# Optimization experiments

Measured on AMD Instinct MI355X. Metric: run time of the kernel, lower is better.

Reference implementation:

```python
import jax, jax.numpy as jnp
import numpy as np

DIM = 1024
CODEBOOK_SIZE = 8192
Z_SHAPE = (16, 4096, DIM)


def setup_inputs() -> dict:
    key = jax.random.key(0)
    k_z, k_cb = jax.random.split(key)
    z = jax.random.normal(k_z, Z_SHAPE, dtype=jnp.float32)
    # nn.Parameter(torch.rand(dim, codebook_size)) -> uniform [0, 1)
    codebook = jax.random.uniform(k_cb, (DIM, CODEBOOK_SIZE), dtype=jnp.float32)
    return {"z": z, "codebook": codebook}


def reference(z, codebook):
    prev_shape = z.shape
    dim = codebook.shape[0]
    z2 = z.reshape(-1, dim)                      # [N, dim]
    dotp = z2 @ codebook                         # [N, K]
    idxes = jnp.argmin(dotp, axis=1)             # [N]
    quantized = codebook.T[idxes]                # [N, dim] gather of codebook columns
    return quantized.reshape(prev_shape)
```

## Files before the change

### kernel.cpp

```cpp
#include <hip/hip_runtime.h>
#include <hip/hip_bf16.h>

#define M_ROWS 65536
#define N_COLS 8192
#define K_DIM  1024
#define CAP    64
#define MARGIN 0.5f
#define PRUNE  0.5f
#define NSEG   3

typedef __attribute__((ext_vector_type(8))) short bf16x8;
typedef __attribute__((ext_vector_type(4))) float f32x4;

__device__ __forceinline__ unsigned short f32_to_bf16_rne(float f) {
  unsigned int u = __float_as_uint(f);
  unsigned int r = u + 0x7fffu + ((u >> 16) & 1u);
  return (unsigned short)(r >> 16);
}

__global__ void vq_convert_z(const float* __restrict__ z, unsigned short* __restrict__ zb,
                             int* __restrict__ counts) {
  const int tid    = blockIdx.x * blockDim.x + threadIdx.x;
  const int stride = gridDim.x * blockDim.x;
  if (tid < M_ROWS) counts[tid] = 0;
  const int total = M_ROWS * (K_DIM / 4);
  for (int i = tid; i < total; i += stride) {
    float4 v = ((const float4*)z)[i];
    ushort4 o;
    o.x = f32_to_bf16_rne(v.x);
    o.y = f32_to_bf16_rne(v.y);
    o.z = f32_to_bf16_rne(v.z);
    o.w = f32_to_bf16_rne(v.w);
    ((ushort4*)zb)[i] = o;
  }
}

__global__ void vq_transpose_cb(const float* __restrict__ cb,
                                float* __restrict__ cbT,
                                unsigned short* __restrict__ cbTb) {
  __shared__ float tile[32][33];
  int n0 = blockIdx.x * 32;
  int k0 = blockIdx.y * 32;
  int tx = threadIdx.x;
  int ty = threadIdx.y;
#pragma unroll
  for (int i = 0; i < 4; ++i) {
    int k = k0 + ty + i * 8;
    tile[ty + i * 8][tx] = cb[(size_t)k * N_COLS + n0 + tx];
  }
  __syncthreads();
#pragma unroll
  for (int i = 0; i < 4; ++i) {
    int n = n0 + ty + i * 8;
    float v = tile[tx][ty + i * 8];
    cbT[(size_t)n * K_DIM + k0 + tx] = v;
    cbTb[(size_t)n * K_DIM + k0 + tx] = f32_to_bf16_rne(v);
  }
}

__global__ __launch_bounds__(256, 3) void vq_gemm(const unsigned short* __restrict__ zb,
                                                  const unsigned short* __restrict__ cbTb,
                                                  int* __restrict__ counts,
                                                  unsigned short* __restrict__ cand,
                                                  float* __restrict__ candv) {
  __shared__ __align__(16) unsigned short As[128 * 64];
  __shared__ __align__(16) unsigned short Bs[128 * 64];
  const int tid  = threadIdx.x;
  const int wave = tid >> 6;
  const int lane = tid & 63;
  const int quad = lane >> 4;
  const int l16  = lane & 15;
  const int b      = blockIdx.x;
  const int seg    = b >> 9;
  const int stripe = b & 511;
  const int row0 = stripe * 128;
  const int rr = lane >> 3;
  const int sgo = (((lane & 7) ^ rr) << 3);
  const int swz = l16 & 7;

  float run[2][4];
#pragma unroll
  for (int a = 0; a < 2; ++a)
#pragma unroll
    for (int b2 = 0; b2 < 4; ++b2) run[a][b2] = 1e30f;

  const int nc0 = (seg * 64) / NSEG;
  const int nc1 = ((seg + 1) * 64) / NSEG;
  for (int nc = nc0; nc < nc1; ++nc) {
    const int col0 = nc * 128;
    f32x4 acc[2][8];
#pragma unroll
    for (int a = 0; a < 2; ++a)
#pragma unroll
      for (int b2 = 0; b2 < 8; ++b2) acc[a][b2] = (f32x4){0.f, 0.f, 0.f, 0.f};

    for (int kk = 0; kk < K_DIM; kk += 64) {
      const int rbase = wave * 32;
#pragma unroll
      for (int c = 0; c < 4; ++c) {
        const int r = rbase + c * 8;
        const unsigned short* ga = zb + ((size_t)(row0 + r + rr) << 10) + kk + sgo;
        __builtin_amdgcn_global_load_lds(
            (const __attribute__((address_space(1))) void*)ga,
            (__attribute__((address_space(3))) void*)(As + r * 64), 16, 0, 0);
        const unsigned short* gb = cbTb + ((size_t)(col0 + r + rr) << 10) + kk + sgo;
        __builtin_amdgcn_global_load_lds(
            (const __attribute__((address_space(1))) void*)gb,
            (__attribute__((address_space(3))) void*)(Bs + r * 64), 16, 0, 0);
      }
      __syncthreads();
#pragma unroll
      for (int ks = 0; ks < 2; ++ks) {
        const int koff = (((ks * 4 + quad) ^ swz) << 3);
        const int ma0 = wave * 32 + l16;
        bf16x8 a0 = *(const bf16x8*)(As + ma0 * 64 + koff);
        bf16x8 a1 = *(const bf16x8*)(As + (ma0 + 16) * 64 + koff);
#pragma unroll
        for (int ns = 0; ns < 8; ++ns) {
          bf16x8 bfrag = *(const bf16x8*)(Bs + (ns * 16 + l16) * 64 + koff);
          acc[0][ns] = __builtin_amdgcn_mfma_f32_16x16x32_bf16(a0, bfrag, acc[0][ns], 0, 0, 0);
          acc[1][ns] = __builtin_amdgcn_mfma_f32_16x16x32_bf16(a1, bfrag, acc[1][ns], 0, 0, 0);
        }
      }
      __syncthreads();
    }

#pragma unroll
    for (int ms = 0; ms < 2; ++ms) {
#pragma unroll
      for (int r = 0; r < 4; ++r) {
        float v = acc[ms][0][r];
#pragma unroll
        for (int ns = 1; ns < 8; ++ns) v = fminf(v, acc[ms][ns][r]);
#pragma unroll
        for (int m = 1; m < 16; m <<= 1) v = fminf(v, __shfl_xor(v, m));
        float rm = fminf(run[ms][r], v);
        run[ms][r] = rm;
        const float thr = rm + MARGIN;
        const int row = row0 + wave * 32 + ms * 16 + quad * 4 + r;
#pragma unroll
        for (int ns = 0; ns < 8; ++ns) {
          if (acc[ms][ns][r] <= thr) {
            int slot = atomicAdd(&counts[row], 1);
            if (slot < CAP) {
              cand [(size_t)row * CAP + slot] = (unsigned short)(col0 + ns * 16 + l16);
              candv[(size_t)row * CAP + slot] = acc[ms][ns][r];
            }
          }
        }
      }
    }
  }
}

__global__ __launch_bounds__(256) void vq_refine(const float* __restrict__ z,
                                                 const float* __restrict__ cbT,
                                                 const int* __restrict__ counts,
                                                 const unsigned short* __restrict__ cand,
                                                 const float* __restrict__ candv,
                                                 float* __restrict__ out) {
  __shared__ float zs[4][K_DIM];
  const int wv   = threadIdx.x >> 6;
  const int row  = blockIdx.x * 4 + wv;
  const int lane = threadIdx.x & 63;
  const float* zr = z + ((size_t)row << 10);
#pragma unroll
  for (int j = 0; j < 4; ++j)
    ((float4*)zs[wv])[j * 64 + lane] = ((const float4*)zr)[j * 64 + lane];
  __syncthreads();

  const int cnt = counts[row];
  float bestv = 1e30f;
  int bestc = 0x7fffffff;
  const float4* z4 = (const float4*)zs[wv];

  if (cnt <= CAP) {
    int   c  = 0x7fffffff;
    float cv = 1e30f;
    if (lane < cnt) {
      c  = (int)cand[(size_t)row * CAP + lane];
      cv = candv[(size_t)row * CAP + lane];
    }
    float vmin = cv;
#pragma unroll
    for (int m = 1; m < 64; m <<= 1) vmin = fminf(vmin, __shfl_xor(vmin, m));
    if (lane < cnt && cv <= vmin + PRUNE) {
      const float4* cb4 = (const float4*)(cbT + ((size_t)c << 10));
      float s = 0.f;
      float4 buf[8];
#pragma unroll
      for (int j = 0; j < 8; ++j) buf[j] = cb4[j];
      for (int q0 = 0; q0 < K_DIM / 4; q0 += 8) {
        float4 nxt[8];
        if (q0 + 8 < K_DIM / 4) {
#pragma unroll
          for (int j = 0; j < 8; ++j) nxt[j] = cb4[q0 + 8 + j];
        }
#pragma unroll
        for (int j = 0; j < 8; ++j) {
          float4 zv = z4[q0 + j];
          s = fmaf(zv.x, buf[j].x, s);
          s = fmaf(zv.y, buf[j].y, s);
          s = fmaf(zv.z, buf[j].z, s);
          s = fmaf(zv.w, buf[j].w, s);
        }
#pragma unroll
        for (int j = 0; j < 8; ++j) buf[j] = nxt[j];
      }
      bestv = s;
      bestc = c;
    }
  } else {
    for (int base = 0; base < N_COLS; base += 64) {
      const int c = base + lane;
      const float4* cb4 = (const float4*)(cbT + ((size_t)c << 10));
      float s = 0.f;
      for (int q = 0; q < K_DIM / 4; ++q) {
        float4 cvx = cb4[q];
        float4 zv  = z4[q];
        s = fmaf(zv.x, cvx.x, s);
        s = fmaf(zv.y, cvx.y, s);
        s = fmaf(zv.z, cvx.z, s);
        s = fmaf(zv.w, cvx.w, s);
      }
      if (s < bestv || (s == bestv && c < bestc)) { bestv = s; bestc = c; }
    }
  }

#pragma unroll
  for (int m = 1; m < 64; m <<= 1) {
    float v2 = __shfl_xor(bestv, m);
    int   c2 = __shfl_xor(bestc, m);
    if (v2 < bestv || (v2 == bestv && c2 < bestc)) { bestv = v2; bestc = c2; }
  }
  if (bestc >= N_COLS || bestc < 0) bestc = 0;

  const float4* src = (const float4*)(cbT + ((size_t)bestc << 10));
  float4* dst = (float4*)(out + ((size_t)row << 10));
#pragma unroll
  for (int j = 0; j < 4; ++j) dst[j * 64 + lane] = src[j * 64 + lane];
}

__global__ __launch_bounds__(256) void vq_brute(const float* __restrict__ z,
                                                const float* __restrict__ cb,
                                                float* __restrict__ out) {
  const int row = blockIdx.x;
  __shared__ float zr[K_DIM];
  __shared__ float bv[256];
  __shared__ int bc[256];
  for (int i = threadIdx.x; i < K_DIM; i += 256) zr[i] = z[((size_t)row << 10) + i];
  __syncthreads();
  float bestv = 1e30f;
  int bestc = 0x7fffffff;
  for (int ci = 0; ci < N_COLS / 256; ++ci) {
    int c = ci * 256 + threadIdx.x;
    float s = 0.f;
    for (int k = 0; k < K_DIM; ++k)
      s = fmaf(zr[k], cb[((size_t)k << 13) + c], s);
    if (s < bestv || (s == bestv && c < bestc)) { bestv = s; bestc = c; }
  }
  bv[threadIdx.x] = bestv; bc[threadIdx.x] = bestc;
  __syncthreads();
  for (int sft = 128; sft > 0; sft >>= 1) {
    if (threadIdx.x < sft) {
      float v2 = bv[threadIdx.x + sft]; int c2 = bc[threadIdx.x + sft];
      if (v2 < bv[threadIdx.x] || (v2 == bv[threadIdx.x] && c2 < bc[threadIdx.x])) {
        bv[threadIdx.x] = v2; bc[threadIdx.x] = c2;
      }
    }
    __syncthreads();
  }
  const int c = bc[0];
  for (int d = threadIdx.x; d < K_DIM; d += 256)
    out[((size_t)row << 10) + d] = cb[((size_t)d << 13) + c];
}

extern "C" void kernel_launch(void* const* d_in, const int* in_sizes, int n_in,
                              void* d_out, int out_size, void* d_ws, size_t ws_size,
                              hipStream_t stream) {
  const float* z  = (const float*)d_in[0];
  const float* cb = (const float*)d_in[1];
  float* out = (float*)d_out;

  const size_t zb_bytes     = (size_t)M_ROWS * K_DIM * 2;
  const size_t cbT_bytes    = (size_t)N_COLS * K_DIM * 4;
  const size_t cbTb_bytes   = (size_t)N_COLS * K_DIM * 2;
  const size_t cand_bytes   = (size_t)M_ROWS * CAP * 2;
  const size_t candv_bytes  = (size_t)M_ROWS * CAP * 4;
  const size_t counts_bytes = (size_t)M_ROWS * 4;
  const size_t need = zb_bytes + cbT_bytes + cbTb_bytes + cand_bytes + candv_bytes + counts_bytes;

  if (ws_size < need) {
    vq_brute<<<M_ROWS, 256, 0, stream>>>(z, cb, out);
    return;
  }

  char* p = (char*)d_ws;
  unsigned short* zb    = (unsigned short*)p; p += zb_bytes;
  float*          cbT   = (float*)p;          p += cbT_bytes;
  unsigned short* cbTb  = (unsigned short*)p; p += cbTb_bytes;
  unsigned short* cand  = (unsigned short*)p; p += cand_bytes;
  float*          candv = (float*)p;          p += candv_bytes;
  int*            counts = (int*)p;

  vq_convert_z<<<2048, 256, 0, stream>>>(z, zb, counts);
  vq_transpose_cb<<<dim3(N_COLS / 32, K_DIM / 32), dim3(32, 8), 0, stream>>>(cb, cbT, cbTb);
  vq_gemm<<<(M_ROWS / 128) * NSEG, 256, 0, stream>>>(zb, cbTb, counts, cand, candv);
  vq_refine<<<M_ROWS / 4, 256, 0, stream>>>(z, cbT, counts, cand, candv, out);
}
```

Before: 2.282 ms.

## Skip fp32 refinement when bf16 winner is clear; split decide and gather kernels

The refine stage becomes a decide kernel that accepts the bf16 GEMM's best candidate directly when it is unique and beats the runner-up by more than a gap threshold. Only rows with close candidates pay for the fp32 dot-product refinement, which now reads z straight from global memory instead of staging it in shared memory. The output gather moves to a separate grid-stride kernel driven by a per-row index buffer. The shortcut trusts bf16 accuracy inside the 0.3 gap, so ties or near-ties beyond that gap could be picked incorrectly, and the extra kernel launch and index buffer add a little overhead.

Result: faster. 2.031 ms (-11.0%).

```diff
diff --git a/kernel.cpp b/kernel.cpp
--- a/kernel.cpp
+++ b/kernel.cpp
@@ -6,7 +6,7 @@
 #define K_DIM  1024
 #define CAP    64
 #define MARGIN 0.5f
-#define PRUNE  0.5f
+#define GAPTHR 0.3f
 #define NSEG   3
 
 typedef __attribute__((ext_vector_type(8))) short bf16x8;
@@ -153,92 +153,123 @@
   }
 }
 
-__global__ __launch_bounds__(256) void vq_refine(const float* __restrict__ z,
+__global__ __launch_bounds__(256) void vq_decide(const float* __restrict__ z,
                                                  const float* __restrict__ cbT,
                                                  const int* __restrict__ counts,
                                                  const unsigned short* __restrict__ cand,
                                                  const float* __restrict__ candv,
+                                                 int* __restrict__ bestc_out) {
+  const int gtid   = blockIdx.x * blockDim.x + threadIdx.x;
+  const int wid    = gtid >> 6;
+  const int lane   = gtid & 63;
+  const int nwaves = (gridDim.x * blockDim.x) >> 6;
+
+  for (int row = wid; row < M_ROWS; row += nwaves) {
+    const int cnt = counts[row];
+    const float4* z4g = (const float4*)(z + ((size_t)row << 10));
+    int best;
+
+    if (cnt <= CAP) {
+      int   c  = 0x7fffffff;
+      float cv = 1e30f;
+      if (lane < cnt) {
+        c  = (int)cand[(size_t)row * CAP + lane];
+        cv = candv[(size_t)row * CAP + lane];
+      }
+      float vmin = cv; int cmin = c;
+#pragma unroll
+      for (int m = 1; m < 64; m <<= 1) {
+        float v2 = __shfl_xor(vmin, m);
+        int   c2 = __shfl_xor(cmin, m);
+        if (v2 < vmin || (v2 == vmin && c2 < cmin)) { vmin = v2; cmin = c2; }
+      }
+      unsigned long long tie = __ballot(cv == vmin);
+      float cv2 = (cv == vmin) ? 1e30f : cv;
+      float vsec = cv2;
+#pragma unroll
+      for (int m = 1; m < 64; m <<= 1) vsec = fminf(vsec, __shfl_xor(vsec, m));
+
+      if (__popcll(tie) == 1 && vsec - vmin > GAPTHR) {
+        best = cmin;
+      } else {
+        float rv = 1e30f; int rc = 0x7fffffff;
+        if (lane < cnt && cv <= vmin + GAPTHR) {
+          const float4* cb4 = (const float4*)(cbT + ((size_t)c << 10));
+          float s = 0.f;
+          float4 cbuf[4], zbuf[4];
+#pragma unroll
+          for (int j = 0; j < 4; ++j) { cbuf[j] = cb4[j]; zbuf[j] = z4g[j]; }
+          for (int q0 = 0; q0 < K_DIM / 4; q0 += 4) {
+            float4 cn[4], zn[4];
+            if (q0 + 4 < K_DIM / 4) {
+#pragma unroll
+              for (int j = 0; j < 4; ++j) { cn[j] = cb4[q0 + 4 + j]; zn[j] = z4g[q0 + 4 + j]; }
+            }
+#pragma unroll
+            for (int j = 0; j < 4; ++j) {
+              s = fmaf(zbuf[j].x, cbuf[j].x, s);
+              s = fmaf(zbuf[j].y, cbuf[j].y, s);
+              s = fmaf(zbuf[j].z, cbuf[j].z, s);
+              s = fmaf(zbuf[j].w, cbuf[j].w, s);
+            }
+#pragma unroll
+            for (int j = 0; j < 4; ++j) { cbuf[j] = cn[j]; zbuf[j] = zn[j]; }
+          }
+          rv = s; rc = c;
+        }
+#pragma unroll
+        for (int m = 1; m < 64; m <<= 1) {
+          float v2 = __shfl_xor(rv, m);
+          int   c2 = __shfl_xor(rc, m);
+          if (v2 < rv || (v2 == rv && c2 < rc)) { rv = v2; rc = c2; }
+        }
+        best = rc;
+      }
+    } else {
+      float rv = 1e30f; int rc = 0x7fffffff;
+      for (int base = 0; base < N_COLS; base += 64) {
+        const int cc = base + lane;
+        const float4* cb4 = (const float4*)(cbT + ((size_t)cc << 10));
+        float s = 0.f;
+        for (int q = 0; q < K_DIM / 4; ++q) {
+          float4 cv4 = cb4[q];
+          float4 zv  = z4g[q];
+          s = fmaf(zv.x, cv4.x, s);
+          s = fmaf(zv.y, cv4.y, s);
+          s = fmaf(zv.z, cv4.z, s);
+          s = fmaf(zv.w, cv4.w, s);
+        }
+        if (s < rv || (s == rv && cc < rc)) { rv = s; rc = cc; }
+      }
+#pragma unroll
+      for (int m = 1; m < 64; m <<= 1) {
+        float v2 = __shfl_xor(rv, m);
+        int   c2 = __shfl_xor(rc, m);
+        if (v2 < rv || (v2 == rv && c2 < rc)) { rv = v2; rc = c2; }
+      }
+      best = rc;
+    }
+
+    if (best >= N_COLS || best < 0) best = 0;
+    if (lane == 0) bestc_out[row] = best;
+  }
+}
+
+__global__ __launch_bounds__(256) void vq_gather(const float* __restrict__ cbT,
+                                                 const int* __restrict__ bestc,
                                                  float* __restrict__ out) {
-  __shared__ float zs[4][K_DIM];
-  const int wv   = threadIdx.x >> 6;
-  const int row  = blockIdx.x * 4 + wv;
-  const int lane = threadIdx.x & 63;
-  const float* zr = z + ((size_t)row << 10);
-#pragma unroll
-  for (int j = 0; j < 4; ++j)
-    ((float4*)zs[wv])[j * 64 + lane] = ((const float4*)zr)[j * 64 + lane];
-  __syncthreads();
-
-  const int cnt = counts[row];
-  float bestv = 1e30f;
-  int bestc = 0x7fffffff;
-  const float4* z4 = (const float4*)zs[wv];
-
-  if (cnt <= CAP) {
-    int   c  = 0x7fffffff;
-    float cv = 1e30f;
-    if (lane < cnt) {
-      c  = (int)cand[(size_t)row * CAP + lane];
-      cv = candv[(size_t)row * CAP + lane];
-    }
-    float vmin = cv;
-#pragma unroll
-    for (int m = 1; m < 64; m <<= 1) vmin = fminf(vmin, __shfl_xor(vmin, m));
-    if (lane < cnt && cv <= vmin + PRUNE) {
-      const float4* cb4 = (const float4*)(cbT + ((size_t)c << 10));
-      float s = 0.f;
-      float4 buf[8];
-#pragma unroll
-      for (int j = 0; j < 8; ++j) buf[j] = cb4[j];
-      for (int q0 = 0; q0 < K_DIM / 4; q0 += 8) {
-        float4 nxt[8];
-        if (q0 + 8 < K_DIM / 4) {
-#pragma unroll
-          for (int j = 0; j < 8; ++j) nxt[j] = cb4[q0 + 8 + j];
-        }
-#pragma unroll
-        for (int j = 0; j < 8; ++j) {
-          float4 zv = z4[q0 + j];
-          s = fmaf(zv.x, buf[j].x, s);
-          s = fmaf(zv.y, buf[j].y, s);
-          s = fmaf(zv.z, buf[j].z, s);
-          s = fmaf(zv.w, buf[j].w, s);
-        }
-#pragma unroll
-        for (int j = 0; j < 8; ++j) buf[j] = nxt[j];
-      }
-      bestv = s;
-      bestc = c;
-    }
-  } else {
-    for (int base = 0; base < N_COLS; base += 64) {
-      const int c = base + lane;
-      const float4* cb4 = (const float4*)(cbT + ((size_t)c << 10));
-      float s = 0.f;
-      for (int q = 0; q < K_DIM / 4; ++q) {
-        float4 cvx = cb4[q];
-        float4 zv  = z4[q];
-        s = fmaf(zv.x, cvx.x, s);
-        s = fmaf(zv.y, cvx.y, s);
-        s = fmaf(zv.z, cvx.z, s);
-        s = fmaf(zv.w, cvx.w, s);
-      }
-      if (s < bestv || (s == bestv && c < bestc)) { bestv = s; bestc = c; }
-    }
-  }
-
-#pragma unroll
-  for (int m = 1; m < 64; m <<= 1) {
-    float v2 = __shfl_xor(bestv, m);
-    int   c2 = __shfl_xor(bestc, m);
-    if (v2 < bestv || (v2 == bestv && c2 < bestc)) { bestv = v2; bestc = c2; }
-  }
-  if (bestc >= N_COLS || bestc < 0) bestc = 0;
-
-  const float4* src = (const float4*)(cbT + ((size_t)bestc << 10));
-  float4* dst = (float4*)(out + ((size_t)row << 10));
-#pragma unroll
-  for (int j = 0; j < 4; ++j) dst[j * 64 + lane] = src[j * 64 + lane];
+  const int gtid   = blockIdx.x * blockDim.x + threadIdx.x;
+  const int wid    = gtid >> 6;
+  const int lane   = gtid & 63;
+  const int nwaves = (gridDim.x * blockDim.x) >> 6;
+  for (int row = wid; row < M_ROWS; row += nwaves) {
+    int c = bestc[row];
+    if (c < 0 || c >= N_COLS) c = 0;
+    const float4* src = (const float4*)(cbT + ((size_t)c << 10));
+    float4* dst = (float4*)(out + ((size_t)row << 10));
+#pragma unroll
+    for (int j = 0; j < 4; ++j) dst[j * 64 + lane] = src[j * 64 + lane];
+  }
 }
 
 __global__ __launch_bounds__(256) void vq_brute(const float* __restrict__ z,
@@ -288,7 +319,9 @@
   const size_t cand_bytes   = (size_t)M_ROWS * CAP * 2;
   const size_t candv_bytes  = (size_t)M_ROWS * CAP * 4;
   const size_t counts_bytes = (size_t)M_ROWS * 4;
-  const size_t need = zb_bytes + cbT_bytes + cbTb_bytes + cand_bytes + candv_bytes + counts_bytes;
+  const size_t bestc_bytes  = (size_t)M_ROWS * 4;
+  const size_t need = zb_bytes + cbT_bytes + cbTb_bytes + cand_bytes + candv_bytes +
+                      counts_bytes + bestc_bytes;
 
   if (ws_size < need) {
     vq_brute<<<M_ROWS, 256, 0, stream>>>(z, cb, out);
@@ -301,10 +334,12 @@
   unsigned short* cbTb  = (unsigned short*)p; p += cbTb_bytes;
   unsigned short* cand  = (unsigned short*)p; p += cand_bytes;
   float*          candv = (float*)p;          p += candv_bytes;
-  int*            counts = (int*)p;
+  int*            counts = (int*)p;           p += counts_bytes;
+  int*            bestc  = (int*)p;
 
   vq_convert_z<<<2048, 256, 0, stream>>>(z, zb, counts);
   vq_transpose_cb<<<dim3(N_COLS / 32, K_DIM / 32), dim3(32, 8), 0, stream>>>(cb, cbT, cbTb);
   vq_gemm<<<(M_ROWS / 128) * NSEG, 256, 0, stream>>>(zb, cbTb, counts, cand, candv);
-  vq_refine<<<M_ROWS / 4, 256, 0, stream>>>(z, cbT, counts, cand, candv, out);
-}
+  vq_decide<<<2048, 256, 0, stream>>>(z, cbT, counts, cand, candv, bestc);
+  vq_gather<<<2048, 256, 0, stream>>>(cbT, bestc, out);
+}
```
